# Kernel optimization log

Measured on AMD Instinct MI355X. Metric: run time of the kernel, lower is better.

The kernel has to match this reference:

```python
import jax, jax.numpy as jnp
import numpy as np

B, S, D, F, E, DT, K = 4, 2048, 1024, 4096, 8, 256, 2


def setup_inputs() -> dict:
    key = jax.random.key(0)
    ks = jax.random.split(key, 8)
    scale_g = 1.0 / np.sqrt(D)
    scale_t = 1.0 / np.sqrt(DT)
    scale_1 = 1.0 / np.sqrt(D)
    scale_2 = 1.0 / np.sqrt(F)
    return {
        "inputs": jax.random.normal(ks[0], (B, S, D), dtype=jnp.float32),
        "task_param": jax.random.normal(ks[1], (B, 1, DT), dtype=jnp.float32),
        "Wg_in": jax.random.normal(ks[2], (D, E), dtype=jnp.float32) * scale_g,
        "bg_in": jnp.zeros((E,), dtype=jnp.float32),
        "Wg_task": jax.random.normal(ks[3], (DT, E), dtype=jnp.float32) * scale_t,
        "bg_task": jnp.zeros((E,), dtype=jnp.float32),
        "alpha": jnp.float32(0.5),
        "W1": jax.random.normal(ks[4], (E, D, F), dtype=jnp.float32) * scale_1,
        "b1": jnp.zeros((E, F), dtype=jnp.float32),
        "W2": jax.random.normal(ks[5], (E, F, D), dtype=jnp.float32) * scale_2,
        "b2": jnp.zeros((E, D), dtype=jnp.float32),
    }


def reference(inputs, task_param, Wg_in, bg_in, Wg_task, bg_task, alpha, W1, b1, W2, b2):
    # Gating: blend input-gate and task-gate logits ([B,1,E] broadcasts over S)
    input_logits = jnp.einsum('bsd,de->bse', inputs, Wg_in) + bg_in
    task_logits = jnp.einsum('btd,de->bte', task_param, Wg_task) + bg_task
    gate_logits = (1.0 - alpha) * input_logits + alpha * task_logits  # [B,S,E]

    topk_vals, selected = jax.lax.top_k(gate_logits, K)  # [B,S,K]

    # Load-balancing auxiliary loss (float32 softmax, as in the original)
    weights_softmax = jax.nn.softmax(gate_logits.astype(jnp.float32), axis=-1).astype(inputs.dtype)
    average_weight = jnp.mean(weights_softmax, axis=(0, 1))  # [E]
    onehot = jax.nn.one_hot(selected, E, dtype=inputs.dtype)  # [B,S,K,E]
    average_count = jnp.mean(onehot.sum(axis=2), axis=(0, 1))  # [E]
    l_aux = jnp.mean(average_weight * average_count) * E

    # Combine weights: softmax over the top-k gate values
    w = jax.nn.softmax(topk_vals.astype(jnp.float32), axis=-1).astype(inputs.dtype)  # [B,S,K]

    # Dense expert compute (same math as the per-expert gather/scatter loop)
    h = jax.nn.silu(jnp.einsum('bsd,edf->ebsf', inputs, W1) + b1[:, None, None, :])  # [E,B,S,F]
    expert_out = jnp.einsum('ebsf,efd->ebsd', h, W2) + b2[:, None, None, :]          # [E,B,S,D]

    picked = jnp.einsum('bske,ebsd->bskd', onehot, expert_out)  # [B,S,K,D]
    results = jnp.einsum('bsk,bskd->bsd', w, picked)            # [B,S,D]
    return results, l_aux.astype(jnp.float32)
```

## Files before the change

### kernel.cpp

```cpp
#include <hip/hip_runtime.h>

#define T_TOK 8192
#define D_DIM 1024
#define F_DIM 4096
#define E_EXP 8
#define DT_DIM 256
#define GBLK 256

#define A_XB   0u
#define A_WT   16777216u
#define A_H    83886080u
#define A_Y    226492416u
#define A_META 262144000u
#define MO_FILL   0
#define MO_PB     64
#define MO_NT     128
#define MO_PARTP  256
#define MO_PARTC  8448
#define MO_TILEE  16640
#define MO_TILERB 17664
#define MO_ROUTEE 18688
#define MO_ROUTEW 84224
#define MO_TSLOT  149760
#define MO_PTOK   215296
#define META_BYTES 284928
#define META_INTS  (META_BYTES/4)

using bf16x8 = __attribute__((ext_vector_type(8))) short;
using f32x4  = __attribute__((ext_vector_type(4))) float;
typedef unsigned short u16;

__device__ __forceinline__ u16 f2bf(float f) {
  union { float f; unsigned u; } v; v.f = f;
  unsigned r = v.u + 0x7FFFu + ((v.u >> 16) & 1u);
  return (u16)(r >> 16);
}
__device__ __forceinline__ float bf2f(u16 h) {
  union { unsigned u; float f; } v; v.u = ((unsigned)h) << 16; return v.f;
}
__device__ __forceinline__ void gload16(const void* gsrc, void* ldst) {
  __builtin_amdgcn_global_load_lds(
      (const __attribute__((address_space(1))) void*)gsrc,
      (__attribute__((address_space(3))) void*)ldst, 16, 0, 0);
}

__global__ void zerok(int* p, int n) {
  int i = blockIdx.x * 256 + threadIdx.x;
  if (i < n) p[i] = 0;
}

__global__ __launch_bounds__(256) void tcvt(const float* __restrict__ src,
                                            u16* __restrict__ dst, int R, int C) {
  __shared__ u16 tile[32][33];
  size_t off = (size_t)blockIdx.z * R * C;
  int cb = blockIdx.x * 32, rb = blockIdx.y * 32;
  int tx = threadIdx.x & 31, ty = threadIdx.x >> 5;
#pragma unroll
  for (int i = 0; i < 4; i++)
    tile[ty + i * 8][tx] = f2bf(src[off + (size_t)(rb + ty + i * 8) * C + cb + tx]);
  __syncthreads();
#pragma unroll
  for (int i = 0; i < 4; i++)
    dst[off + (size_t)(cb + ty + i * 8) * R + rb + tx] = tile[tx][ty + i * 8];
}

__global__ __launch_bounds__(256) void gating(
    const float* __restrict__ X, const float* __restrict__ TP,
    const float* __restrict__ Wg, const float* __restrict__ bg,
    const float* __restrict__ Wt, const float* __restrict__ bgt,
    const float* __restrict__ alphaP, u16* __restrict__ Xb, int* meta) {
  __shared__ float WgT[E_EXP * D_DIM];
  __shared__ float WtT[E_EXP * DT_DIM];
  __shared__ float wsP[4][8];
  __shared__ int   wsC[4][8];
  int tid = threadIdx.x;
  for (int i = tid; i < E_EXP * D_DIM; i += 256) { int d = i >> 3, e = i & 7; WgT[e * D_DIM + d] = Wg[i]; }
  for (int i = tid; i < E_EXP * DT_DIM; i += 256) { int d = i >> 3, e = i & 7; WtT[e * DT_DIM + d] = Wt[i]; }
  __syncthreads();
  int lane = tid & 63, wid = tid >> 6;
  int tb = blockIdx.x * 32;
  int b = tb >> 11;
  float alpha = alphaP[0];

  float tac[8] = {};
#pragma unroll
  for (int i = 0; i < 4; i++) {
    int d = lane + i * 64;
    float x = TP[b * DT_DIM + d];
#pragma unroll
    for (int e = 0; e < 8; e++) tac[e] += x * WtT[e * DT_DIM + d];
  }
  for (int off = 32; off > 0; off >>= 1)
#pragma unroll
    for (int e = 0; e < 8; e++) tac[e] += __shfl_xor(tac[e], off);
  float tl[8];
#pragma unroll
  for (int e = 0; e < 8; e++) tl[e] = alpha * (tac[e] + bgt[e]);

  float psum[8] = {};
  int   cnt[8] = {};
  for (int i = 0; i < 8; i++) {
    int t = tb + wid * 8 + i;
    const float* xr = X + (size_t)t * D_DIM;
    float acc[8] = {};
    u16 xb[16];
#pragma unroll 4
    for (int j = 0; j < 16; j++) {
      int d = lane + j * 64;
      float x = xr[d];
      xb[j] = f2bf(x);
#pragma unroll
      for (int e = 0; e < 8; e++) acc[e] += x * WgT[e * D_DIM + d];
    }
#pragma unroll
    for (int j = 0; j < 16; j++) Xb[(size_t)t * D_DIM + lane + j * 64] = xb[j];
    for (int off = 32; off > 0; off >>= 1)
#pragma unroll
      for (int e = 0; e < 8; e++) acc[e] += __shfl_xor(acc[e], off);
    float gl[8];
#pragma unroll
    for (int e = 0; e < 8; e++) gl[e] = (1.f - alpha) * (acc[e] + bg[e]) + tl[e];
    int e1 = 0;
#pragma unroll
    for (int e = 1; e < 8; e++) if (gl[e] > gl[e1]) e1 = e;
    int es = (e1 == 0) ? 1 : 0;
#pragma unroll
    for (int e = 0; e < 8; e++) if (e != e1 && gl[e] > gl[es]) es = e;
    float mx = gl[0];
#pragma unroll
    for (int e = 1; e < 8; e++) mx = fmaxf(mx, gl[e]);
    float pe[8], se = 0.f;
#pragma unroll
    for (int e = 0; e < 8; e++) { pe[e] = __expf(gl[e] - mx); se += pe[e]; }
    float inv = 1.f / se;
    if (lane == 0) {
#pragma unroll
      for (int e = 0; e < 8; e++) psum[e] += pe[e] * inv;
      cnt[e1]++; cnt[es]++;
      float w1 = 1.f / (1.f + __expf(gl[es] - gl[e1]));
      meta[MO_ROUTEE / 4 + 2 * t] = e1;
      meta[MO_ROUTEE / 4 + 2 * t + 1] = es;
      ((float*)meta)[MO_ROUTEW / 4 + 2 * t] = w1;
      ((float*)meta)[MO_ROUTEW / 4 + 2 * t + 1] = 1.f - w1;
    }
  }
  if (lane == 0) {
#pragma unroll
    for (int e = 0; e < 8; e++) { wsP[wid][e] = psum[e]; wsC[wid][e] = cnt[e]; }
  }
  __syncthreads();
  if (tid < 8) {
    float p = wsP[0][tid] + wsP[1][tid] + wsP[2][tid] + wsP[3][tid];
    int   c = wsC[0][tid] + wsC[1][tid] + wsC[2][tid] + wsC[3][tid];
    ((float*)meta)[MO_PARTP / 4 + blockIdx.x * 8 + tid] = p;
    meta[MO_PARTC / 4 + blockIdx.x * 8 + tid] = c;
  }
}

__global__ void plan(int* meta, float* out) {
  __shared__ float sp[8];
  __shared__ int   sc[8];
  int tid = threadIdx.x;
  if (blockIdx.x != 0) return;
  if (tid < 8) {
    const float* pp = (const float*)meta + MO_PARTP / 4;
    const int*   pc = meta + MO_PARTC / 4;
    float p = 0.f; int c = 0;
    for (int b = 0; b < GBLK; b++) { p += pp[b * 8 + tid]; c += pc[b * 8 + tid]; }
    sp[tid] = p; sc[tid] = c;
  }
  __syncthreads();
  if (tid == 0) {
    int* pb = meta + MO_PB / 4;
    int* tileE = meta + MO_TILEE / 4;
    int* tileRB = meta + MO_TILERB / 4;
    int base = 0, nt = 0;
    float la = 0.f;
    for (int e = 0; e < 8; e++) {
      int n = sc[e];
      pb[e] = base;
      int ntl = (n + 127) >> 7;
      for (int i = 0; i < ntl; i++) { tileE[nt] = e; tileRB[nt] = base + (i << 7); nt++; }
      base += ntl << 7;
      la += (sp[e] * (1.f / 8192.f)) * ((float)n * (1.f / 8192.f));
    }
    pb[8] = base;
    meta[MO_NT / 4] = nt;
    out[T_TOK * D_DIM] = la;
  }
}

__global__ __launch_bounds__(256) void fillk(int* meta) {
  int t = blockIdx.x * 256 + threadIdx.x;
  int lane = threadIdx.x & 63;
  int* pb = meta + MO_PB / 4;
  int* fl = meta + MO_FILL / 4;
  int* ptok = meta + MO_PTOK / 4;
  int* ts = meta + MO_TSLOT / 4;
  unsigned long long lmask = (1ull << lane) - 1;
#pragma unroll
  for (int k = 0; k < 2; k++) {
    int e = meta[MO_ROUTEE / 4 + 2 * t + k];
    int slot = 0;
    for (int ee = 0; ee < 8; ee++) {
      unsigned long long mask = __ballot(e == ee);
      if (e == ee) {
        int low = __ffsll((long long)mask) - 1;
        int pre = __popcll(mask & lmask);
        int base = 0;
        if (lane == low) base = atomicAdd(&fl[ee], __popcll(mask));
        base = __shfl(base, low);
        slot = pb[ee] + base + pre;
      }
    }
    ptok[slot] = t;
    ts[2 * t + k] = slot;
  }
}


__global__ __launch_bounds__(256) void gemm1(
    const u16* __restrict__ Xb, const u16* __restrict__ W1T,
    const float* __restrict__ b1, u16* __restrict__ H, const int* __restrict__ meta) {
  int nt = meta[MO_NT / 4];
  int bt = blockIdx.x;
  if (bt >= nt) return;
  int e = meta[MO_TILEE / 4 + bt];
  int rb = meta[MO_TILERB / 4 + bt];
  int cb = blockIdx.y * 128;
  const int* ptok = meta + MO_PTOK / 4;

  __shared__ short sA[128 * 32];
  __shared__ short sB[128 * 32];
  int tid = threadIdx.x, lane = tid & 63, wid = tid >> 6;
  int wr = wid >> 1, wc = wid & 1;
  int r0 = tid >> 2;
  int c0 = (((tid & 3) ^ ((r0 >> 1) & 3)) << 3);
  int tok0 = ptok[rb + r0];
  int tok1 = ptok[rb + r0 + 64];
  const u16* gA0 = Xb + (size_t)tok0 * D_DIM + c0;
  const u16* gA1 = Xb + (size_t)tok1 * D_DIM + c0;
  const u16* gB0 = W1T + ((size_t)e * F_DIM + cb + r0) * D_DIM + c0;
  const u16* gB1 = gB0 + (size_t)64 * D_DIM;
  char* lA = (char*)sA + wid * 1024;
  char* lB = (char*)sB + wid * 1024;

  f32x4 acc[4][4] = {};
  int kb = (((lane >> 4) ^ (((lane & 15) >> 1) & 3)) << 3);
  for (int k0 = 0; k0 < D_DIM; k0 += 32) {
    __syncthreads();
    gload16(gA0 + k0, lA);
    gload16(gA1 + k0, lA + 4096);
    gload16(gB0 + k0, lB);
    gload16(gB1 + k0, lB + 4096);
    __syncthreads();
    bf16x8 af[4], bfr[4];
    int ra = wr * 64 + (lane & 15);
#pragma unroll
    for (int m = 0; m < 4; m++)
      af[m] = *(const bf16x8*)((const char*)sA + ((ra + m * 16) * 32 + kb) * 2);
    int rn = wc * 64 + (lane & 15);
#pragma unroll
    for (int n = 0; n < 4; n++)
      bfr[n] = *(const bf16x8*)((const char*)sB + ((rn + n * 16) * 32 + kb) * 2);
#pragma unroll
    for (int m = 0; m < 4; m++)
#pragma unroll
      for (int n = 0; n < 4; n++)
        acc[m][n] = __builtin_amdgcn_mfma_f32_16x16x32_bf16(af[m], bfr[n], acc[m][n], 0, 0, 0);
  }
  int rbase = wr * 64 + ((lane >> 4) << 2);
  int cbase = cb + wc * 64 + (lane & 15);
#pragma unroll
  for (int m = 0; m < 4; m++)
#pragma unroll
    for (int n = 0; n < 4; n++) {
      int f = cbase + n * 16;
      float bias = b1[e * F_DIM + f];
#pragma unroll
      for (int r = 0; r < 4; r++) {
        int p = rb + rbase + m * 16 + r;
        float v = acc[m][n][r] + bias;
        float s = v * (1.0f / (1.0f + __expf(-v)));
        H[(size_t)p * F_DIM + f] = f2bf(s);
      }
    }
}

__global__ __launch_bounds__(256) void gemm2(
    const u16* __restrict__ H, const u16* __restrict__ W2T,
    const float* __restrict__ b2, u16* __restrict__ Y, const int* __restrict__ meta) {
  int id = blockIdx.x;
  int wg = (id & 7) * 136 + (id >> 3);
  int bt = wg >> 3;
  int cb = (wg & 7) * 128;
  int nt = meta[MO_NT / 4];
  if (bt >= nt) return;
  int e = meta[MO_TILEE / 4 + bt];
  int rb = meta[MO_TILERB / 4 + bt];
  __shared__ short sA[128 * 32];
  __shared__ short sB[128 * 32];
  int tid = threadIdx.x, lane = tid & 63, wid = tid >> 6;
  int wr = wid >> 1, wc = wid & 1;
  int r0 = tid >> 2;
  int c0 = (((tid & 3) ^ ((r0 >> 1) & 3)) << 3);
  const u16* gA0 = H + (size_t)(rb + r0) * F_DIM + c0;
  const u16* gA1 = gA0 + (size_t)64 * F_DIM;
  const u16* gB0 = W2T + ((size_t)e * D_DIM + cb + r0) * F_DIM + c0;
  const u16* gB1 = gB0 + (size_t)64 * F_DIM;
  char* lA = (char*)sA + wid * 1024;
  char* lB = (char*)sB + wid * 1024;

  f32x4 acc[4][4] = {};
  int kb = (((lane >> 4) ^ (((lane & 15) >> 1) & 3)) << 3);
  for (int k0 = 0; k0 < F_DIM; k0 += 32) {
    __syncthreads();
    gload16(gA0 + k0, lA);
    gload16(gA1 + k0, lA + 4096);
    gload16(gB0 + k0, lB);
    gload16(gB1 + k0, lB + 4096);
    __syncthreads();
    bf16x8 af[4], bfr[4];
    int ra = wr * 64 + (lane & 15);
#pragma unroll
    for (int m = 0; m < 4; m++)
      af[m] = *(const bf16x8*)((const char*)sA + ((ra + m * 16) * 32 + kb) * 2);
    int rn = wc * 64 + (lane & 15);
#pragma unroll
    for (int n = 0; n < 4; n++)
      bfr[n] = *(const bf16x8*)((const char*)sB + ((rn + n * 16) * 32 + kb) * 2);
#pragma unroll
    for (int m = 0; m < 4; m++)
#pragma unroll
      for (int n = 0; n < 4; n++)
        acc[m][n] = __builtin_amdgcn_mfma_f32_16x16x32_bf16(af[m], bfr[n], acc[m][n], 0, 0, 0);
  }
  int rbase = wr * 64 + ((lane >> 4) << 2);
  int cbase = cb + wc * 64 + (lane & 15);
#pragma unroll
  for (int m = 0; m < 4; m++)
#pragma unroll
    for (int n = 0; n < 4; n++) {
      int d = cbase + n * 16;
      float bias = b2[e * D_DIM + d];
#pragma unroll
      for (int r = 0; r < 4; r++) {
        int p = rb + rbase + m * 16 + r;
        Y[(size_t)p * D_DIM + d] = f2bf(acc[m][n][r] + bias);
      }
    }
}

__global__ __launch_bounds__(256) void combine(const u16* __restrict__ Y,
                                               const int* __restrict__ meta,
                                               float* __restrict__ out) {
  int t = blockIdx.x;
  const int* ts = meta + MO_TSLOT / 4;
  const float* rw = (const float*)meta + MO_ROUTEW / 4;
  int s1 = ts[2 * t], s2 = ts[2 * t + 1];
  float w1 = rw[2 * t], w2 = rw[2 * t + 1];
  int d0 = threadIdx.x * 4;
  ushort4 a = *(const ushort4*)(Y + (size_t)s1 * D_DIM + d0);
  ushort4 b = *(const ushort4*)(Y + (size_t)s2 * D_DIM + d0);
  float4 v;
  v.x = w1 * bf2f(a.x) + w2 * bf2f(b.x);
  v.y = w1 * bf2f(a.y) + w2 * bf2f(b.y);
  v.z = w1 * bf2f(a.z) + w2 * bf2f(b.z);
  v.w = w1 * bf2f(a.w) + w2 * bf2f(b.w);
  *(float4*)(out + (size_t)t * D_DIM + d0) = v;
}

extern "C" void kernel_launch(void* const* d_in, const int* in_sizes, int n_in,
                              void* d_out, int out_size, void* d_ws, size_t ws_size,
                              hipStream_t stream) {
  (void)in_sizes; (void)n_in; (void)out_size; (void)ws_size;
  const float* X    = (const float*)d_in[0];
  const float* TP   = (const float*)d_in[1];
  const float* Wg   = (const float*)d_in[2];
  const float* bg   = (const float*)d_in[3];
  const float* Wt   = (const float*)d_in[4];
  const float* bgt  = (const float*)d_in[5];
  const float* alp  = (const float*)d_in[6];
  const float* W1   = (const float*)d_in[7];
  const float* b1   = (const float*)d_in[8];
  const float* W2   = (const float*)d_in[9];
  const float* b2   = (const float*)d_in[10];
  float* out = (float*)d_out;
  char* ws = (char*)d_ws;
  u16* Xb = (u16*)(ws + A_XB);
  u16* WT = (u16*)(ws + A_WT);
  u16* H  = (u16*)(ws + A_H);
  u16* Y  = (u16*)(ws + A_Y);
  int* meta = (int*)(ws + A_META);

  zerok<<<(META_INTS + 255) / 256, 256, 0, stream>>>(meta, META_INTS);
  tcvt<<<dim3(F_DIM / 32, D_DIM / 32, E_EXP), 256, 0, stream>>>(W1, WT, D_DIM, F_DIM);
  gating<<<GBLK, 256, 0, stream>>>(X, TP, Wg, bg, Wt, bgt, alp, Xb, meta);
  plan<<<1, 64, 0, stream>>>(meta, out);
  fillk<<<T_TOK / 256, 256, 0, stream>>>(meta);
  gemm1<<<dim3(136, F_DIM / 128), 256, 0, stream>>>(Xb, WT, b1, H, meta);
  tcvt<<<dim3(D_DIM / 32, F_DIM / 32, E_EXP), 256, 0, stream>>>(W2, WT, F_DIM, D_DIM);
  gemm2<<<1088, 256, 0, stream>>>(H, WT, b2, Y, meta);
  combine<<<T_TOK, 256, 0, stream>>>(Y, meta, out);
}
```

Before: 618.7 us.

## Double-buffer LDS in expert GEMMs and remap gemm1 blocks per XCD

Both expert GEMMs now use two LDS buffers: the global-to-LDS loads for the next K slice are issued right after the barrier, so they overlap the MFMA work on the current slice, and the loop needs one barrier per step instead of two. MFMA sections are wrapped in s_setprio to favour the compute wave. gemm1 switches to a 1D grid whose block index is decoded so that blocks landing on the same XCD share a row tile and a contiguous span of F columns, to improve L2 reuse of the gathered activations. The cost is twice the LDS per block, which may lower occupancy, and an explicit full vmcnt wait each iteration.

```diff
diff --git a/kernel.cpp b/kernel.cpp
--- a/kernel.cpp
+++ b/kernel.cpp
@@ -222,16 +222,17 @@
 __global__ __launch_bounds__(256) void gemm1(
     const u16* __restrict__ Xb, const u16* __restrict__ W1T,
     const float* __restrict__ b1, u16* __restrict__ H, const int* __restrict__ meta) {
+  int xcd = blockIdx.x & 7, loc = blockIdx.x >> 3;
+  int bt = loc >> 2;
+  int cb = (xcd * 4 + (loc & 3)) * 128;
   int nt = meta[MO_NT / 4];
-  int bt = blockIdx.x;
   if (bt >= nt) return;
   int e = meta[MO_TILEE / 4 + bt];
   int rb = meta[MO_TILERB / 4 + bt];
-  int cb = blockIdx.y * 128;
   const int* ptok = meta + MO_PTOK / 4;
 
-  __shared__ short sA[128 * 32];
-  __shared__ short sB[128 * 32];
+  __shared__ short sA[2][128 * 32];
+  __shared__ short sB[2][128 * 32];
   int tid = threadIdx.x, lane = tid & 63, wid = tid >> 6;
   int wr = wid >> 1, wc = wid & 1;
   int r0 = tid >> 2;
@@ -242,32 +243,42 @@
   const u16* gA1 = Xb + (size_t)tok1 * D_DIM + c0;
   const u16* gB0 = W1T + ((size_t)e * F_DIM + cb + r0) * D_DIM + c0;
   const u16* gB1 = gB0 + (size_t)64 * D_DIM;
-  char* lA = (char*)sA + wid * 1024;
-  char* lB = (char*)sB + wid * 1024;
+
+#define STAGE_G1(buf, k0)                                              \
+  {                                                                    \
+    gload16(gA0 + (k0), (char*)&sA[buf][0] + wid * 1024);              \
+    gload16(gA1 + (k0), (char*)&sA[buf][0] + 4096 + wid * 1024);       \
+    gload16(gB0 + (k0), (char*)&sB[buf][0] + wid * 1024);              \
+    gload16(gB1 + (k0), (char*)&sB[buf][0] + 4096 + wid * 1024);       \
+  }
 
   f32x4 acc[4][4] = {};
   int kb = (((lane >> 4) ^ (((lane & 15) >> 1) & 3)) << 3);
+  int ra = wr * 64 + (lane & 15);
+  int rn = wc * 64 + (lane & 15);
+  STAGE_G1(0, 0)
   for (int k0 = 0; k0 < D_DIM; k0 += 32) {
-    __syncthreads();
-    gload16(gA0 + k0, lA);
-    gload16(gA1 + k0, lA + 4096);
-    gload16(gB0 + k0, lB);
-    gload16(gB1 + k0, lB + 4096);
-    __syncthreads();
+    int c = (k0 >> 5) & 1;
+    asm volatile("s_waitcnt vmcnt(0) lgkmcnt(0)" ::: "memory");
+    __builtin_amdgcn_sched_barrier(0);
+    __builtin_amdgcn_s_barrier();
+    if (k0 + 32 < D_DIM) STAGE_G1(c ^ 1, k0 + 32)
+    const short* pA = &sA[c][0];
+    const short* pB = &sB[c][0];
     bf16x8 af[4], bfr[4];
-    int ra = wr * 64 + (lane & 15);
 #pragma unroll
     for (int m = 0; m < 4; m++)
-      af[m] = *(const bf16x8*)((const char*)sA + ((ra + m * 16) * 32 + kb) * 2);
-    int rn = wc * 64 + (lane & 15);
+      af[m] = *(const bf16x8*)((const char*)pA + ((ra + m * 16) * 32 + kb) * 2);
 #pragma unroll
     for (int n = 0; n < 4; n++)
-      bfr[n] = *(const bf16x8*)((const char*)sB + ((rn + n * 16) * 32 + kb) * 2);
+      bfr[n] = *(const bf16x8*)((const char*)pB + ((rn + n * 16) * 32 + kb) * 2);
+    __builtin_amdgcn_s_setprio(1);
 #pragma unroll
     for (int m = 0; m < 4; m++)
 #pragma unroll
       for (int n = 0; n < 4; n++)
         acc[m][n] = __builtin_amdgcn_mfma_f32_16x16x32_bf16(af[m], bfr[n], acc[m][n], 0, 0, 0);
+    __builtin_amdgcn_s_setprio(0);
   }
   int rbase = wr * 64 + ((lane >> 4) << 2);
   int cbase = cb + wc * 64 + (lane & 15);
@@ -298,8 +309,8 @@
   if (bt >= nt) return;
   int e = meta[MO_TILEE / 4 + bt];
   int rb = meta[MO_TILERB / 4 + bt];
-  __shared__ short sA[128 * 32];
-  __shared__ short sB[128 * 32];
+  __shared__ short sA[2][128 * 32];
+  __shared__ short sB[2][128 * 32];
   int tid = threadIdx.x, lane = tid & 63, wid = tid >> 6;
   int wr = wid >> 1, wc = wid & 1;
   int r0 = tid >> 2;
@@ -308,32 +319,42 @@
   const u16* gA1 = gA0 + (size_t)64 * F_DIM;
   const u16* gB0 = W2T + ((size_t)e * D_DIM + cb + r0) * F_DIM + c0;
   const u16* gB1 = gB0 + (size_t)64 * F_DIM;
-  char* lA = (char*)sA + wid * 1024;
-  char* lB = (char*)sB + wid * 1024;
+
+#define STAGE_G2(buf, k0)                                              \
+  {                                                                    \
+    gload16(gA0 + (k0), (char*)&sA[buf][0] + wid * 1024);              \
+    gload16(gA1 + (k0), (char*)&sA[buf][0] + 4096 + wid * 1024);       \
+    gload16(gB0 + (k0), (char*)&sB[buf][0] + wid * 1024);              \
+    gload16(gB1 + (k0), (char*)&sB[buf][0] + 4096 + wid * 1024);       \
+  }
 
   f32x4 acc[4][4] = {};
   int kb = (((lane >> 4) ^ (((lane & 15) >> 1) & 3)) << 3);
+  int ra = wr * 64 + (lane & 15);
+  int rn = wc * 64 + (lane & 15);
+  STAGE_G2(0, 0)
   for (int k0 = 0; k0 < F_DIM; k0 += 32) {
-    __syncthreads();
-    gload16(gA0 + k0, lA);
-    gload16(gA1 + k0, lA + 4096);
-    gload16(gB0 + k0, lB);
-    gload16(gB1 + k0, lB + 4096);
-    __syncthreads();
+    int c = (k0 >> 5) & 1;
+    asm volatile("s_waitcnt vmcnt(0) lgkmcnt(0)" ::: "memory");
+    __builtin_amdgcn_sched_barrier(0);
+    __builtin_amdgcn_s_barrier();
+    if (k0 + 32 < F_DIM) STAGE_G2(c ^ 1, k0 + 32)
+    const short* pA = &sA[c][0];
+    const short* pB = &sB[c][0];
     bf16x8 af[4], bfr[4];
-    int ra = wr * 64 + (lane & 15);
 #pragma unroll
     for (int m = 0; m < 4; m++)
-      af[m] = *(const bf16x8*)((const char*)sA + ((ra + m * 16) * 32 + kb) * 2);
-    int rn = wc * 64 + (lane & 15);
+      af[m] = *(const bf16x8*)((const char*)pA + ((ra + m * 16) * 32 + kb) * 2);
 #pragma unroll
     for (int n = 0; n < 4; n++)
-      bfr[n] = *(const bf16x8*)((const char*)sB + ((rn + n * 16) * 32 + kb) * 2);
+      bfr[n] = *(const bf16x8*)((const char*)pB + ((rn + n * 16) * 32 + kb) * 2);
+    __builtin_amdgcn_s_setprio(1);
 #pragma unroll
     for (int m = 0; m < 4; m++)
 #pragma unroll
       for (int n = 0; n < 4; n++)
         acc[m][n] = __builtin_amdgcn_mfma_f32_16x16x32_bf16(af[m], bfr[n], acc[m][n], 0, 0, 0);
+    __builtin_amdgcn_s_setprio(0);
   }
   int rbase = wr * 64 + ((lane >> 4) << 2);
   int cbase = cb + wc * 64 + (lane & 15);
@@ -398,7 +419,7 @@
   gating<<<GBLK, 256, 0, stream>>>(X, TP, Wg, bg, Wt, bgt, alp, Xb, meta);
   plan<<<1, 64, 0, stream>>>(meta, out);
   fillk<<<T_TOK / 256, 256, 0, stream>>>(meta);
-  gemm1<<<dim3(136, F_DIM / 128), 256, 0, stream>>>(Xb, WT, b1, H, meta);
+  gemm1<<<4352, 256, 0, stream>>>(Xb, WT, b1, H, meta);
   tcvt<<<dim3(D_DIM / 32, F_DIM / 32, E_EXP), 256, 0, stream>>>(W2, WT, F_DIM, D_DIM);
   gemm2<<<1088, 256, 0, stream>>>(H, WT, b2, Y, meta);
   combine<<<T_TOK, 256, 0, stream>>>(Y, meta, out);
```

Result: faster. 588.2 us (-4.9%).
